# Kernel tuning notes

Hardware: AMD Instinct MI355X
Metric: run time of the kernel (lower is better)

The kernel has to match this reference:

```python
import jax, jax.numpy as jnp
import numpy as np

NUM_PARTS = 8
NUM_KP = 32768
BETA_DIM = 64
NUM_JOINTS = NUM_PARTS - 1
REG_WEIGHT = 0.001


def setup_inputs() -> dict:
    key = jax.random.key(0)
    ks = jax.random.split(key, 9)
    return {
        "pred_kp": jax.random.normal(ks[0], (NUM_PARTS, NUM_KP, 3), jnp.float32),
        "base_r_quat": jax.random.normal(ks[1], (4,), jnp.float32),
        "base_t": jax.random.normal(ks[2], (1, 3), jnp.float32),
        "joint_state": jax.random.normal(ks[3], (NUM_JOINTS,), jnp.float32),
        "beta": jax.random.normal(ks[4], (1, BETA_DIM), jnp.float32),
        "part_kp_weight": jax.random.uniform(ks[5], (NUM_PARTS, NUM_KP), jnp.float32),
        "W_kp": jax.random.normal(ks[6], (BETA_DIM, NUM_PARTS, NUM_KP, 3), jnp.float32) * 0.05,
        "W_loc": jax.random.normal(ks[7], (BETA_DIM, NUM_JOINTS, 3), jnp.float32) * 0.1,
        "W_axis": jax.random.normal(ks[8], (BETA_DIM, NUM_JOINTS, 3), jnp.float32) * 0.1,
    }


def reference(pred_kp, base_r_quat, base_t, joint_state, beta, part_kp_weight, W_kp, W_loc, W_axis):
    sg = jax.lax.stop_gradient
    # Stand-in for model.get_norm_keypoints / get_norm_joint_params: linear in beta.
    norm_kp = jnp.einsum('be,epkd->pkd', beta, W_kp)            # [P, K, 3]
    joint_loc = jnp.einsum('be,ejd->jd', beta, W_loc)           # [J, 3]
    joint_axis = jnp.einsum('be,ejd->jd', beta, W_axis)         # [J, 3]
    joint_axis = joint_axis / jnp.linalg.norm(joint_axis, axis=-1, keepdims=True)

    homo_norm_kp = jnp.concatenate([norm_kp, jnp.ones(norm_kp.shape[:-1] + (1,), norm_kp.dtype)], -1)   # [P,K,4]
    homo_pred_kp = jnp.concatenate([pred_kp, jnp.ones(pred_kp.shape[:-1] + (1,), pred_kp.dtype)], -1)   # [P,K,4]

    # quaternion (w,x,y,z) -> rotation matrix
    q = base_r_quat / jnp.linalg.norm(base_r_quat)
    a, b, c, d = q[0], q[1], q[2], q[3]
    R = jnp.stack([1 - 2*c*c - 2*d*d, 2*b*c - 2*a*d, 2*a*c + 2*b*d,
                   2*b*c + 2*a*d, 1 - 2*b*b - 2*d*d, 2*c*d - 2*a*b,
                   2*b*d - 2*a*c, 2*a*b + 2*c*d, 1 - 2*b*b - 2*c*c]).reshape(3, 3)
    bottom = jnp.array([[0.0, 0.0, 0.0, 1.0]], dtype=R.dtype)
    base_T = jnp.concatenate([jnp.concatenate([R, base_t.T], axis=1), bottom], axis=0)  # [4,4]

    base_obj = jnp.mean(jnp.linalg.norm(homo_norm_kp[0] @ base_T.T - homo_pred_kp[0], axis=-1) * part_kp_weight[0])

    # transform joint anchors / axes into camera frame (vectorized over joints)
    homo_anchor = jnp.concatenate([joint_loc, jnp.ones((NUM_JOINTS, 1), joint_loc.dtype)], axis=-1)  # [J,4]
    new_anchor = (homo_anchor @ base_T.T)[:, :3]   # [J,3]
    new_axis = joint_axis @ R.T                    # [J,3]

    # revolute screw-motion transform about line (anchor, axis), angle = -joint_state
    aa, bb, cc = new_anchor[:, 0], new_anchor[:, 1], new_anchor[:, 2]
    u, v, w = new_axis[:, 0], new_axis[:, 1], new_axis[:, 2]
    cos = jnp.cos(-joint_state)
    sin = jnp.sin(-joint_state)
    omc = 1.0 - cos
    rel = jnp.stack([
        u*u + (v*v + w*w)*cos, u*v*omc - w*sin, u*w*omc + v*sin,
        (aa*(v*v + w*w) - u*(bb*v + cc*w))*omc + (bb*w - cc*v)*sin,
        u*v*omc + w*sin, v*v + (u*u + w*w)*cos, v*w*omc - u*sin,
        (bb*(u*u + w*w) - v*(aa*u + cc*w))*omc + (cc*u - aa*w)*sin,
        u*w*omc - v*sin, v*w*omc + u*sin, w*w + (u*u + v*v)*cos,
        (cc*(u*u + v*v) - w*(aa*u + bb*v))*omc + (aa*v - bb*u)*sin,
    ], axis=-1).reshape(NUM_JOINTS, 3, 4)
    rel = jnp.concatenate([rel, jnp.broadcast_to(bottom, (NUM_JOINTS, 1, 4))], axis=1)  # [J,4,4]

    child_T = jnp.einsum('jab,bc->jac', rel, base_T)                      # [J,4,4]
    transformed = jnp.einsum('jab,jkb->jka', child_T, homo_norm_kp[1:])   # [J,K,4]
    child_obj = jnp.mean(jnp.linalg.norm(transformed - homo_pred_kp[1:], axis=-1) * part_kp_weight[1:], axis=-1)  # [J]

    all_obj = (base_obj + child_obj.sum()) / NUM_PARTS + (beta * beta).mean() * REG_WEIGHT

    new_joint_params = (sg(new_anchor), sg(new_axis))
    norm_joint_params = (sg(joint_loc), sg(joint_axis))
    return (all_obj, sg(base_T), sg(rel), new_joint_params, norm_joint_params, sg(norm_kp))
```

## Files before the change

### kernel.cpp

```cpp
#include <hip/hip_runtime.h>
#include <math.h>

#define NPARTS 8
#define NKP 32768
#define BDIM 64
#define NJ 7
#define NPTS (NPARTS * NKP)
#define WSTRIDE (NPTS * 3)
#define NBLK (NPTS / 128)

#define OFF_OBJ    0
#define OFF_BASET  1
#define OFF_REL    17
#define OFF_NANCH  129
#define OFF_NAXIS  150
#define OFF_JLOC   171
#define OFF_JAXIS  192
#define OFF_NKPOUT 213


__global__ void setup_kernel(const float* __restrict__ quat,
                             const float* __restrict__ base_t,
                             const float* __restrict__ jstate,
                             const float* __restrict__ beta,
                             const float* __restrict__ W_loc,
                             const float* __restrict__ W_axis,
                             float* __restrict__ out,
                             float* __restrict__ allT) {
  int t = threadIdx.x;
  float q0 = quat[0], q1 = quat[1], q2 = quat[2], q3 = quat[3];
  float qn = sqrtf(q0 * q0 + q1 * q1 + q2 * q2 + q3 * q3);
  float a = q0 / qn, b = q1 / qn, c = q2 / qn, d = q3 / qn;
  float R00 = 1.f - 2.f * c * c - 2.f * d * d, R01 = 2.f * b * c - 2.f * a * d,
        R02 = 2.f * a * c + 2.f * b * d;
  float R10 = 2.f * b * c + 2.f * a * d, R11 = 1.f - 2.f * b * b - 2.f * d * d,
        R12 = 2.f * c * d - 2.f * a * b;
  float R20 = 2.f * b * d - 2.f * a * c, R21 = 2.f * a * b + 2.f * c * d,
        R22 = 1.f - 2.f * b * b - 2.f * c * c;
  float t0 = base_t[0], t1 = base_t[1], t2 = base_t[2];
  float T[16] = {R00, R01, R02, t0, R10, R11, R12, t1,
                 R20, R21, R22, t2, 0.f, 0.f, 0.f, 1.f};

  if (t == 7) {
    for (int i = 0; i < 16; i++) {
      out[OFF_BASET + i] = T[i];
      allT[i] = T[i];
    }
  }

  if (t < NJ) {
    int j = t;
    float l0 = 0.f, l1 = 0.f, l2 = 0.f, x0 = 0.f, x1 = 0.f, x2 = 0.f;
    for (int e = 0; e < BDIM; e++) {
      float be = beta[e];
      l0 += be * W_loc[e * 21 + j * 3 + 0];
      l1 += be * W_loc[e * 21 + j * 3 + 1];
      l2 += be * W_loc[e * 21 + j * 3 + 2];
      x0 += be * W_axis[e * 21 + j * 3 + 0];
      x1 += be * W_axis[e * 21 + j * 3 + 1];
      x2 += be * W_axis[e * 21 + j * 3 + 2];
    }
    float xn = sqrtf(x0 * x0 + x1 * x1 + x2 * x2);
    x0 /= xn; x1 /= xn; x2 /= xn;
    out[OFF_JLOC + j * 3 + 0] = l0;
    out[OFF_JLOC + j * 3 + 1] = l1;
    out[OFF_JLOC + j * 3 + 2] = l2;
    out[OFF_JAXIS + j * 3 + 0] = x0;
    out[OFF_JAXIS + j * 3 + 1] = x1;
    out[OFF_JAXIS + j * 3 + 2] = x2;

    float aa = R00 * l0 + R01 * l1 + R02 * l2 + t0;
    float bb = R10 * l0 + R11 * l1 + R12 * l2 + t1;
    float cc = R20 * l0 + R21 * l1 + R22 * l2 + t2;
    float u = R00 * x0 + R01 * x1 + R02 * x2;
    float v = R10 * x0 + R11 * x1 + R12 * x2;
    float w = R20 * x0 + R21 * x1 + R22 * x2;
    out[OFF_NANCH + j * 3 + 0] = aa;
    out[OFF_NANCH + j * 3 + 1] = bb;
    out[OFF_NANCH + j * 3 + 2] = cc;
    out[OFF_NAXIS + j * 3 + 0] = u;
    out[OFF_NAXIS + j * 3 + 1] = v;
    out[OFF_NAXIS + j * 3 + 2] = w;

    float th = jstate[j];
    float cth = cosf(-th), sth = sinf(-th), omc = 1.f - cth;
    float rel[16];
    rel[0] = u * u + (v * v + w * w) * cth;
    rel[1] = u * v * omc - w * sth;
    rel[2] = u * w * omc + v * sth;
    rel[3] = (aa * (v * v + w * w) - u * (bb * v + cc * w)) * omc + (bb * w - cc * v) * sth;
    rel[4] = u * v * omc + w * sth;
    rel[5] = v * v + (u * u + w * w) * cth;
    rel[6] = v * w * omc - u * sth;
    rel[7] = (bb * (u * u + w * w) - v * (aa * u + cc * w)) * omc + (cc * u - aa * w) * sth;
    rel[8] = u * w * omc - v * sth;
    rel[9] = v * w * omc + u * sth;
    rel[10] = w * w + (u * u + v * v) * cth;
    rel[11] = (cc * (u * u + v * v) - w * (aa * u + bb * v)) * omc + (aa * v - bb * u) * sth;
    rel[12] = 0.f; rel[13] = 0.f; rel[14] = 0.f; rel[15] = 1.f;
    for (int i = 0; i < 16; i++) out[OFF_REL + j * 16 + i] = rel[i];

    for (int r = 0; r < 4; r++)
      for (int cix = 0; cix < 4; cix++) {
        float s = 0.f;
        for (int k2 = 0; k2 < 4; k2++) s += rel[r * 4 + k2] * T[k2 * 4 + cix];
        allT[(j + 1) * 16 + r * 4 + cix] = s;
      }
  }
}

__global__ __launch_bounds__(256) void fused_kernel(
    const float* __restrict__ W_kp, const float* __restrict__ beta,
    const float* __restrict__ pred_kp, const float* __restrict__ wgt,
    const float* __restrict__ allT, float* __restrict__ out_nkp,
    float* __restrict__ partials) {
  __shared__ float sb[BDIM];
  __shared__ float Ts[16];
  __shared__ float part[128 * 3];
  __shared__ float red[4];

  int tid = threadIdx.x;
  int idx = tid & 127;
  int h = tid >> 7;
  int p = blockIdx.x * 128 + idx;
  int pid = (blockIdx.x * 128) >> 15;

  if (tid < BDIM) sb[tid] = beta[tid];
  if (tid < 16) Ts[tid] = allT[pid * 16 + tid];
  __syncthreads();

  const float* base = W_kp + (size_t)(h * 32) * WSTRIDE + (size_t)p * 3;
  float ax = 0.f, ay = 0.f, az = 0.f;
#pragma unroll 8
  for (int e = 0; e < 32; e++) {
    float3 vv = *(const float3*)(base + (size_t)e * WSTRIDE);
    float be = sb[h * 32 + e];
    ax = fmaf(be, vv.x, ax);
    ay = fmaf(be, vv.y, ay);
    az = fmaf(be, vv.z, az);
  }

  if (h == 1) {
    part[idx * 3 + 0] = ax;
    part[idx * 3 + 1] = ay;
    part[idx * 3 + 2] = az;
  }
  __syncthreads();

  float v = 0.f;
  if (h == 0) {
    float x = ax + part[idx * 3 + 0];
    float y = ay + part[idx * 3 + 1];
    float z = az + part[idx * 3 + 2];
    float3 o; o.x = x; o.y = y; o.z = z;
    *(float3*)(out_nkp + (size_t)p * 3) = o;

    float3 pk = *(const float3*)(pred_kp + (size_t)p * 3);
    float w = wgt[p];
    float dx = Ts[0] * x + Ts[1] * y + Ts[2]  * z + Ts[3]  - pk.x;
    float dy = Ts[4] * x + Ts[5] * y + Ts[6]  * z + Ts[7]  - pk.y;
    float dz = Ts[8] * x + Ts[9] * y + Ts[10] * z + Ts[11] - pk.z;
    v = sqrtf(dx * dx + dy * dy + dz * dz) * w;
  }
#pragma unroll
  for (int off = 32; off > 0; off >>= 1) v += __shfl_down(v, off, 64);
  if ((tid & 63) == 0) red[tid >> 6] = v;
  __syncthreads();
  if (tid == 0) partials[blockIdx.x] = red[0] + red[1] + red[2] + red[3];
}

__global__ __launch_bounds__(256) void finish_kernel(
    const float* __restrict__ partials, const float* __restrict__ beta,
    float* __restrict__ out_obj) {
  __shared__ float red[4];
  int tid = threadIdx.x;
  float s = 0.f;
#pragma unroll
  for (int k = 0; k < NBLK / 256; k++) s += partials[tid + 256 * k];
#pragma unroll
  for (int off = 32; off > 0; off >>= 1) s += __shfl_down(s, off, 64);
  if ((tid & 63) == 0) red[tid >> 6] = s;
  __syncthreads();
  if (tid == 0) {
    float reg = 0.f;
    for (int e = 0; e < BDIM; e++) {
      float be = beta[e];
      reg += be * be;
    }
    float total = red[0] + red[1] + red[2] + red[3];
    out_obj[0] = total * (1.0f / (float)NPTS) + (reg / (float)BDIM) * 0.001f;
  }
}

extern "C" void kernel_launch(void* const* d_in, const int* in_sizes, int n_in,
                              void* d_out, int out_size, void* d_ws, size_t ws_size,
                              hipStream_t stream) {
  const float* pred_kp = (const float*)d_in[0];
  const float* quat    = (const float*)d_in[1];
  const float* base_t  = (const float*)d_in[2];
  const float* jstate  = (const float*)d_in[3];
  const float* beta    = (const float*)d_in[4];
  const float* wgt     = (const float*)d_in[5];
  const float* W_kp    = (const float*)d_in[6];
  const float* W_loc   = (const float*)d_in[7];
  const float* W_axis  = (const float*)d_in[8];
  float* out      = (float*)d_out;
  float* allT     = (float*)d_ws;
  float* partials = (float*)d_ws + 128;

  setup_kernel<<<1, 64, 0, stream>>>(quat, base_t, jstate, beta, W_loc, W_axis, out, allT);
  fused_kernel<<<NBLK, 256, 0, stream>>>(W_kp, beta, pred_kp, wgt, allT,
                                         out + OFF_NKPOUT, partials);
  finish_kernel<<<1, 256, 0, stream>>>(partials, beta, out);
}
```

Baseline: 47.06 us.

## Fuse setup and finish kernels into single kernel with last-block reduction

```diff
diff --git a/kernel.cpp b/kernel.cpp
--- a/kernel.cpp
+++ b/kernel.cpp
@@ -19,115 +19,128 @@
 #define OFF_NKPOUT 213
 
 
-__global__ void setup_kernel(const float* __restrict__ quat,
-                             const float* __restrict__ base_t,
-                             const float* __restrict__ jstate,
-                             const float* __restrict__ beta,
-                             const float* __restrict__ W_loc,
-                             const float* __restrict__ W_axis,
-                             float* __restrict__ out,
-                             float* __restrict__ allT) {
-  int t = threadIdx.x;
-  float q0 = quat[0], q1 = quat[1], q2 = quat[2], q3 = quat[3];
-  float qn = sqrtf(q0 * q0 + q1 * q1 + q2 * q2 + q3 * q3);
-  float a = q0 / qn, b = q1 / qn, c = q2 / qn, d = q3 / qn;
-  float R00 = 1.f - 2.f * c * c - 2.f * d * d, R01 = 2.f * b * c - 2.f * a * d,
-        R02 = 2.f * a * c + 2.f * b * d;
-  float R10 = 2.f * b * c + 2.f * a * d, R11 = 1.f - 2.f * b * b - 2.f * d * d,
-        R12 = 2.f * c * d - 2.f * a * b;
-  float R20 = 2.f * b * d - 2.f * a * c, R21 = 2.f * a * b + 2.f * c * d,
-        R22 = 1.f - 2.f * b * b - 2.f * c * c;
-  float t0 = base_t[0], t1 = base_t[1], t2 = base_t[2];
-  float T[16] = {R00, R01, R02, t0, R10, R11, R12, t1,
-                 R20, R21, R22, t2, 0.f, 0.f, 0.f, 1.f};
-
-  if (t == 7) {
-    for (int i = 0; i < 16; i++) {
-      out[OFF_BASET + i] = T[i];
-      allT[i] = T[i];
-    }
-  }
-
-  if (t < NJ) {
-    int j = t;
-    float l0 = 0.f, l1 = 0.f, l2 = 0.f, x0 = 0.f, x1 = 0.f, x2 = 0.f;
-    for (int e = 0; e < BDIM; e++) {
-      float be = beta[e];
-      l0 += be * W_loc[e * 21 + j * 3 + 0];
-      l1 += be * W_loc[e * 21 + j * 3 + 1];
-      l2 += be * W_loc[e * 21 + j * 3 + 2];
-      x0 += be * W_axis[e * 21 + j * 3 + 0];
-      x1 += be * W_axis[e * 21 + j * 3 + 1];
-      x2 += be * W_axis[e * 21 + j * 3 + 2];
-    }
-    float xn = sqrtf(x0 * x0 + x1 * x1 + x2 * x2);
-    x0 /= xn; x1 /= xn; x2 /= xn;
-    out[OFF_JLOC + j * 3 + 0] = l0;
-    out[OFF_JLOC + j * 3 + 1] = l1;
-    out[OFF_JLOC + j * 3 + 2] = l2;
-    out[OFF_JAXIS + j * 3 + 0] = x0;
-    out[OFF_JAXIS + j * 3 + 1] = x1;
-    out[OFF_JAXIS + j * 3 + 2] = x2;
-
-    float aa = R00 * l0 + R01 * l1 + R02 * l2 + t0;
-    float bb = R10 * l0 + R11 * l1 + R12 * l2 + t1;
-    float cc = R20 * l0 + R21 * l1 + R22 * l2 + t2;
-    float u = R00 * x0 + R01 * x1 + R02 * x2;
-    float v = R10 * x0 + R11 * x1 + R12 * x2;
-    float w = R20 * x0 + R21 * x1 + R22 * x2;
-    out[OFF_NANCH + j * 3 + 0] = aa;
-    out[OFF_NANCH + j * 3 + 1] = bb;
-    out[OFF_NANCH + j * 3 + 2] = cc;
-    out[OFF_NAXIS + j * 3 + 0] = u;
-    out[OFF_NAXIS + j * 3 + 1] = v;
-    out[OFF_NAXIS + j * 3 + 2] = w;
-
-    float th = jstate[j];
-    float cth = cosf(-th), sth = sinf(-th), omc = 1.f - cth;
-    float rel[16];
-    rel[0] = u * u + (v * v + w * w) * cth;
-    rel[1] = u * v * omc - w * sth;
-    rel[2] = u * w * omc + v * sth;
-    rel[3] = (aa * (v * v + w * w) - u * (bb * v + cc * w)) * omc + (bb * w - cc * v) * sth;
-    rel[4] = u * v * omc + w * sth;
-    rel[5] = v * v + (u * u + w * w) * cth;
-    rel[6] = v * w * omc - u * sth;
-    rel[7] = (bb * (u * u + w * w) - v * (aa * u + cc * w)) * omc + (cc * u - aa * w) * sth;
-    rel[8] = u * w * omc - v * sth;
-    rel[9] = v * w * omc + u * sth;
-    rel[10] = w * w + (u * u + v * v) * cth;
-    rel[11] = (cc * (u * u + v * v) - w * (aa * u + bb * v)) * omc + (aa * v - bb * u) * sth;
-    rel[12] = 0.f; rel[13] = 0.f; rel[14] = 0.f; rel[15] = 1.f;
-    for (int i = 0; i < 16; i++) out[OFF_REL + j * 16 + i] = rel[i];
-
-    for (int r = 0; r < 4; r++)
-      for (int cix = 0; cix < 4; cix++) {
-        float s = 0.f;
-        for (int k2 = 0; k2 < 4; k2++) s += rel[r * 4 + k2] * T[k2 * 4 + cix];
-        allT[(j + 1) * 16 + r * 4 + cix] = s;
-      }
-  }
-}
-
-__global__ __launch_bounds__(256) void fused_kernel(
+__global__ __launch_bounds__(256) void fused_all(
     const float* __restrict__ W_kp, const float* __restrict__ beta,
     const float* __restrict__ pred_kp, const float* __restrict__ wgt,
-    const float* __restrict__ allT, float* __restrict__ out_nkp,
-    float* __restrict__ partials) {
+    const float* __restrict__ quat, const float* __restrict__ base_t,
+    const float* __restrict__ jstate, const float* __restrict__ W_loc,
+    const float* __restrict__ W_axis, float* __restrict__ out,
+    float* __restrict__ partials, unsigned int* __restrict__ counter) {
   __shared__ float sb[BDIM];
   __shared__ float Ts[16];
   __shared__ float part[128 * 3];
   __shared__ float red[4];
-
-  int tid = threadIdx.x;
-  int idx = tid & 127;
-  int h = tid >> 7;
-  int p = blockIdx.x * 128 + idx;
-  int pid = (blockIdx.x * 128) >> 15;
+  __shared__ int lastflag;
+
+  const int tid = threadIdx.x;
+  const int bid = blockIdx.x;
+  const int pid = bid >> 8;
 
   if (tid < BDIM) sb[tid] = beta[tid];
-  if (tid < 16) Ts[tid] = allT[pid * 16 + tid];
-  __syncthreads();
+
+  if (tid < 64) {
+    float q0 = quat[0], q1 = quat[1], q2 = quat[2], q3 = quat[3];
+    float qn = sqrtf(q0 * q0 + q1 * q1 + q2 * q2 + q3 * q3);
+    float a = q0 / qn, b = q1 / qn, c = q2 / qn, d = q3 / qn;
+    float R00 = 1.f - 2.f * c * c - 2.f * d * d, R01 = 2.f * b * c - 2.f * a * d,
+          R02 = 2.f * a * c + 2.f * b * d;
+    float R10 = 2.f * b * c + 2.f * a * d, R11 = 1.f - 2.f * b * b - 2.f * d * d,
+          R12 = 2.f * c * d - 2.f * a * b;
+    float R20 = 2.f * b * d - 2.f * a * c, R21 = 2.f * a * b + 2.f * c * d,
+          R22 = 1.f - 2.f * b * b - 2.f * c * c;
+    float t0 = base_t[0], t1 = base_t[1], t2 = base_t[2];
+    float T[16] = {R00, R01, R02, t0, R10, R11, R12, t1,
+                   R20, R21, R22, t2, 0.f, 0.f, 0.f, 1.f};
+
+    const bool write_small = (bid >= 1 && bid <= NJ);
+    const bool need_joint = (pid > 0) || write_small;
+
+    if (need_joint) {
+      const int j = (pid > 0) ? (pid - 1) : (bid - 1);
+      float be = beta[tid];
+      float l0 = be * W_loc[tid * 21 + j * 3 + 0];
+      float l1 = be * W_loc[tid * 21 + j * 3 + 1];
+      float l2 = be * W_loc[tid * 21 + j * 3 + 2];
+      float x0 = be * W_axis[tid * 21 + j * 3 + 0];
+      float x1 = be * W_axis[tid * 21 + j * 3 + 1];
+      float x2 = be * W_axis[tid * 21 + j * 3 + 2];
+#pragma unroll
+      for (int off = 32; off > 0; off >>= 1) {
+        l0 += __shfl_xor(l0, off, 64);
+        l1 += __shfl_xor(l1, off, 64);
+        l2 += __shfl_xor(l2, off, 64);
+        x0 += __shfl_xor(x0, off, 64);
+        x1 += __shfl_xor(x1, off, 64);
+        x2 += __shfl_xor(x2, off, 64);
+      }
+      float xn = sqrtf(x0 * x0 + x1 * x1 + x2 * x2);
+      x0 /= xn; x1 /= xn; x2 /= xn;
+      float aa = R00 * l0 + R01 * l1 + R02 * l2 + t0;
+      float bb = R10 * l0 + R11 * l1 + R12 * l2 + t1;
+      float cc = R20 * l0 + R21 * l1 + R22 * l2 + t2;
+      float u = R00 * x0 + R01 * x1 + R02 * x2;
+      float v = R10 * x0 + R11 * x1 + R12 * x2;
+      float w = R20 * x0 + R21 * x1 + R22 * x2;
+      float th = jstate[j];
+      float cth = cosf(-th), sth = sinf(-th), omc = 1.f - cth;
+      float rel[12];
+      rel[0]  = u * u + (v * v + w * w) * cth;
+      rel[1]  = u * v * omc - w * sth;
+      rel[2]  = u * w * omc + v * sth;
+      rel[3]  = (aa * (v * v + w * w) - u * (bb * v + cc * w)) * omc + (bb * w - cc * v) * sth;
+      rel[4]  = u * v * omc + w * sth;
+      rel[5]  = v * v + (u * u + w * w) * cth;
+      rel[6]  = v * w * omc - u * sth;
+      rel[7]  = (bb * (u * u + w * w) - v * (aa * u + cc * w)) * omc + (cc * u - aa * w) * sth;
+      rel[8]  = u * w * omc - v * sth;
+      rel[9]  = v * w * omc + u * sth;
+      rel[10] = w * w + (u * u + v * v) * cth;
+      rel[11] = (cc * (u * u + v * v) - w * (aa * u + bb * v)) * omc + (aa * v - bb * u) * sth;
+      float C[12];
+#pragma unroll
+      for (int r = 0; r < 3; r++)
+#pragma unroll
+        for (int cx = 0; cx < 4; cx++)
+          C[r * 4 + cx] = rel[r * 4 + 0] * T[0 + cx] + rel[r * 4 + 1] * T[4 + cx] +
+                          rel[r * 4 + 2] * T[8 + cx] + rel[r * 4 + 3] * T[12 + cx];
+      if (tid == 0) {
+        if (pid > 0) {
+          for (int i = 0; i < 12; i++) Ts[i] = C[i];
+          Ts[12] = 0.f; Ts[13] = 0.f; Ts[14] = 0.f; Ts[15] = 1.f;
+        } else {
+          for (int i = 0; i < 16; i++) Ts[i] = T[i];
+        }
+        if (write_small) {
+          out[OFF_JLOC + j * 3 + 0] = l0;
+          out[OFF_JLOC + j * 3 + 1] = l1;
+          out[OFF_JLOC + j * 3 + 2] = l2;
+          out[OFF_JAXIS + j * 3 + 0] = x0;
+          out[OFF_JAXIS + j * 3 + 1] = x1;
+          out[OFF_JAXIS + j * 3 + 2] = x2;
+          out[OFF_NANCH + j * 3 + 0] = aa;
+          out[OFF_NANCH + j * 3 + 1] = bb;
+          out[OFF_NANCH + j * 3 + 2] = cc;
+          out[OFF_NAXIS + j * 3 + 0] = u;
+          out[OFF_NAXIS + j * 3 + 1] = v;
+          out[OFF_NAXIS + j * 3 + 2] = w;
+          for (int i = 0; i < 12; i++) out[OFF_REL + j * 16 + i] = rel[i];
+          out[OFF_REL + j * 16 + 12] = 0.f;
+          out[OFF_REL + j * 16 + 13] = 0.f;
+          out[OFF_REL + j * 16 + 14] = 0.f;
+          out[OFF_REL + j * 16 + 15] = 1.f;
+        }
+      }
+    } else if (tid == 0) {
+      for (int i = 0; i < 16; i++) Ts[i] = T[i];
+      if (bid == 0)
+        for (int i = 0; i < 16; i++) out[OFF_BASET + i] = T[i];
+    }
+  }
+  __syncthreads();
+
+  const int idx = tid & 127;
+  const int h = tid >> 7;
+  const int p = bid * 128 + idx;
 
   const float* base = W_kp + (size_t)(h * 32) * WSTRIDE + (size_t)p * 3;
   float ax = 0.f, ay = 0.f, az = 0.f;
@@ -147,48 +160,51 @@
   }
   __syncthreads();
 
-  float v = 0.f;
+  float vsum = 0.f;
   if (h == 0) {
     float x = ax + part[idx * 3 + 0];
     float y = ay + part[idx * 3 + 1];
     float z = az + part[idx * 3 + 2];
     float3 o; o.x = x; o.y = y; o.z = z;
-    *(float3*)(out_nkp + (size_t)p * 3) = o;
+    *(float3*)(out + OFF_NKPOUT + (size_t)p * 3) = o;
 
     float3 pk = *(const float3*)(pred_kp + (size_t)p * 3);
     float w = wgt[p];
     float dx = Ts[0] * x + Ts[1] * y + Ts[2]  * z + Ts[3]  - pk.x;
     float dy = Ts[4] * x + Ts[5] * y + Ts[6]  * z + Ts[7]  - pk.y;
     float dz = Ts[8] * x + Ts[9] * y + Ts[10] * z + Ts[11] - pk.z;
-    v = sqrtf(dx * dx + dy * dy + dz * dz) * w;
-  }
-#pragma unroll
-  for (int off = 32; off > 0; off >>= 1) v += __shfl_down(v, off, 64);
-  if ((tid & 63) == 0) red[tid >> 6] = v;
-  __syncthreads();
-  if (tid == 0) partials[blockIdx.x] = red[0] + red[1] + red[2] + red[3];
-}
-
-__global__ __launch_bounds__(256) void finish_kernel(
-    const float* __restrict__ partials, const float* __restrict__ beta,
-    float* __restrict__ out_obj) {
-  __shared__ float red[4];
-  int tid = threadIdx.x;
-  float s = 0.f;
-#pragma unroll
-  for (int k = 0; k < NBLK / 256; k++) s += partials[tid + 256 * k];
-#pragma unroll
-  for (int off = 32; off > 0; off >>= 1) s += __shfl_down(s, off, 64);
-  if ((tid & 63) == 0) red[tid >> 6] = s;
-  __syncthreads();
+    vsum = sqrtf(dx * dx + dy * dy + dz * dz) * w;
+  }
+#pragma unroll
+  for (int off = 32; off > 0; off >>= 1) vsum += __shfl_down(vsum, off, 64);
+  if ((tid & 63) == 0) red[tid >> 6] = vsum;
+  __syncthreads();
+
   if (tid == 0) {
-    float reg = 0.f;
-    for (int e = 0; e < BDIM; e++) {
-      float be = beta[e];
-      reg += be * be;
+    float psum = red[0] + red[1] + red[2] + red[3];
+    __hip_atomic_store(&partials[bid], psum, __ATOMIC_RELEASE,
+                       __HIP_MEMORY_SCOPE_AGENT);
+    unsigned int old = __hip_atomic_fetch_add(counter, 1u, __ATOMIC_ACQ_REL,
+                                              __HIP_MEMORY_SCOPE_AGENT);
+    lastflag = (old == NBLK - 1) ? 1 : 0;
+  }
+  __syncthreads();
+  if (lastflag) {
+    float s = 0.f;
+#pragma unroll
+    for (int k = 0; k < NBLK / 256; k++)
+      s += __hip_atomic_load(&partials[tid + 256 * k], __ATOMIC_ACQUIRE,
+                             __HIP_MEMORY_SCOPE_AGENT);
+#pragma unroll
+    for (int off = 32; off > 0; off >>= 1) s += __shfl_down(s, off, 64);
+    if ((tid & 63) == 0) red[tid >> 6] = s;
+    __syncthreads();
+    if (tid == 0) {
+      float reg = 0.f;
+      for (int e = 0; e < BDIM; e++) reg += sb[e] * sb[e];
+      out[OFF_OBJ] = (red[0] + red[1] + red[2] + red[3]) * (1.f / (float)NPTS) +
+                     (reg / (float)BDIM) * 0.001f;
     }
-    float total = red[0] + red[1] + red[2] + red[3];
-    out_obj[0] = total * (1.0f / (float)NPTS) + (reg / (float)BDIM) * 0.001f;
   }
 }
 
@@ -204,12 +220,12 @@
   const float* W_kp    = (const float*)d_in[6];
   const float* W_loc   = (const float*)d_in[7];
   const float* W_axis  = (const float*)d_in[8];
-  float* out      = (float*)d_out;
-  float* allT     = (float*)d_ws;
-  float* partials = (float*)d_ws + 128;
-
-  setup_kernel<<<1, 64, 0, stream>>>(quat, base_t, jstate, beta, W_loc, W_axis, out, allT);
-  fused_kernel<<<NBLK, 256, 0, stream>>>(W_kp, beta, pred_kp, wgt, allT,
-                                         out + OFF_NKPOUT, partials);
-  finish_kernel<<<1, 256, 0, stream>>>(partials, beta, out);
+  float* out = (float*)d_out;
+  float* partials = (float*)d_ws;
+  unsigned int* counter = (unsigned int*)((char*)d_ws + NBLK * sizeof(float));
+
+  hipMemsetAsync(counter, 0, sizeof(unsigned int), stream);
+  fused_all<<<NBLK, 256, 0, stream>>>(W_kp, beta, pred_kp, wgt, quat, base_t,
+                                      jstate, W_loc, W_axis, out, partials,
+                                      counter);
 }
```

Result: slower. 157.7 us (+235.2%).
